# Kernel tuning notes

Hardware: AMD Instinct MI355X
Metric: run time of the kernel (lower is better)

## Reference

```python
import jax, jax.numpy as jnp
import numpy as np

EPS = 1e-5  # BatchNorm eps (torch default); BN is in training mode with gamma=1, beta=0 (init values)


def bn(x, axes):
    m = jnp.mean(x, axis=axes, keepdims=True)
    v = jnp.var(x, axis=axes, keepdims=True)
    return (x - m) * jax.lax.rsqrt(v + EPS)


def knn_idx(xyz, k):
    # brute-force squared-distance matrix [B,N,N], k smallest
    d = jnp.sum((xyz[:, :, None, :] - xyz[:, None, :, :]) ** 2, axis=-1)
    _, idx = jax.lax.top_k(-d, k)
    return idx  # [B,N,k]


def gather(x, idx):
    # x: [B,N,C], idx: [B,N,k] -> [B,N,k,C]
    return jax.vmap(lambda a, i: a[i])(x, idx)


def lse(xyz, features, idx, w):
    nbr_xyz = gather(xyz, idx)                       # [B,N,k,3]
    rel = nbr_xyz - xyz[:, :, None, :]
    dist = jnp.sqrt(jnp.maximum(jnp.sum(rel ** 2, -1, keepdims=True), 1e-12))
    nbr_f = gather(features, idx)                    # [B,N,k,C]
    enc = jnp.concatenate([rel, dist, nbr_f], -1)    # [B,N,k,C+4]
    return jax.nn.relu(bn(jnp.einsum('bnkc,oc->bnko', enc, w), (0, 1, 2)))


def att_pool(x, sw1, sw2, sb2, mw):
    # x: [B,N,k,C]
    h = jax.nn.relu(bn(jnp.einsum('bnkc,oc->bnko', x, sw1), (0, 1, 2)))
    scores = jax.nn.softmax(jnp.einsum('bnkc,oc->bnko', h, sw2) + sb2, axis=2)  # softmax over k
    feat = jnp.sum(x * scores, axis=2)               # [B,N,C]
    return jax.nn.relu(bn(jnp.einsum('bnc,oc->bno', feat, mw), (0, 1)))


def drb(x, w1, w2):
    # in_channels == out_channels -> identity shortcut
    h = jax.nn.relu(bn(jnp.einsum('bnc,oc->bno', x, w1), (0, 1)))
    h = bn(jnp.einsum('bnc,oc->bno', h, w2), (0, 1))
    return jax.nn.relu(h + x)


def setup_inputs() -> dict:
    key = jax.random.key(0)
    B, N, C, K, OUT = 4, 8192, 32, 16, 128
    H = OUT // 2  # 64
    ks = jax.random.split(key, 16)
    s = 0.05
    return {
        'xyz': jax.random.normal(ks[0], (B, N, 3), jnp.float32),
        'features': jax.random.normal(ks[1], (B, N, C), jnp.float32),
        'w_lse1': jax.random.normal(ks[2], (H, C + 4), jnp.float32) * s,
        'w_lse2': jax.random.normal(ks[3], (H, C + 4), jnp.float32) * s,
        'ap1_sw1': jax.random.normal(ks[4], (H, H), jnp.float32) * s,
        'ap1_sw2': jax.random.normal(ks[5], (1, H), jnp.float32) * s,
        'ap1_sb2': jax.random.normal(ks[6], (1,), jnp.float32) * s,
        'ap1_mw': jax.random.normal(ks[7], (H, H), jnp.float32) * s,
        'ap2_sw1': jax.random.normal(ks[8], (H, H), jnp.float32) * s,
        'ap2_sw2': jax.random.normal(ks[9], (1, H), jnp.float32) * s,
        'ap2_sb2': jax.random.normal(ks[10], (1,), jnp.float32) * s,
        'ap2_mw': jax.random.normal(ks[11], (H, H), jnp.float32) * s,
        'drb_w1': jax.random.normal(ks[12], (OUT, OUT), jnp.float32) * s,
        'drb_w2': jax.random.normal(ks[13], (OUT, OUT), jnp.float32) * s,
    }


def reference(xyz, features, w_lse1, w_lse2, ap1_sw1, ap1_sw2, ap1_sb2, ap1_mw,
              ap2_sw1, ap2_sw2, ap2_sb2, ap2_mw, drb_w1, drb_w2):
    K = 16
    idx = knn_idx(xyz, K)  # original calls knn twice on same xyz -> identical indices
    f1 = att_pool(lse(xyz, features, idx, w_lse1), ap1_sw1, ap1_sw2, ap1_sb2, ap1_mw)
    f2 = att_pool(lse(xyz, features, idx, w_lse2), ap2_sw1, ap2_sw2, ap2_sb2, ap2_mw)
    agg = jnp.concatenate([f1, f2], axis=-1)  # [B,N,128]
    return drb(agg, drb_w1, drb_w2)           # [B,N,128]
```

## Files before the change

### kernel.cpp

```cpp
#include <hip/hip_runtime.h>
#include <hip/hip_bf16.h>
#include <hip/hip_fp16.h>
#include <float.h>
#include <math.h>

#define DEVFN __device__ __forceinline__

DEVFN void wavefence() { __builtin_amdgcn_wave_barrier(); }

using half8 = __attribute__((ext_vector_type(8))) _Float16;
using f32x4 = __attribute__((ext_vector_type(4))) float;

namespace {
constexpr int Bq = 4, Nq = 8192, Cq = 32, Kq = 16;
constexpr int PTS = Bq * Nq;
constexpr int CH = 16;
constexpr int CAND = Nq / CH;
constexpr double ROWS = 524288.0;

constexpr int DS_Y = 0, DS_Z = 256, DS_G = 512, DS_H1 = 768, DS_H2 = 1024;

constexpr size_t OFF_KD   = 0;
constexpr size_t OFF_KJ   = (size_t)32 << 20;
constexpr size_t OFF_X    = 0;
constexpr size_t OFF_Z    = (size_t)64 << 20;
constexpr size_t OFF_H1   = 0;
constexpr size_t OFF_H2   = (size_t)16 << 20;
constexpr size_t OFF_GRAW = (size_t)192 << 20;
constexpr size_t OFF_AGG  = (size_t)208 << 20;
constexpr size_t OFF_IDX  = (size_t)224 << 20;
constexpr size_t OFF_DST  = (size_t)226 << 20;
constexpr size_t OFF_MST  = ((size_t)226 << 20) + 10240;
constexpr size_t OFF_BNP  = ((size_t)226 << 20) + 16384;
constexpr size_t WS_NEED  = ((size_t)226 << 20) + 32768;
constexpr size_t FB_GRAW  = (size_t)64 << 20;
constexpr size_t FB_AGG   = (size_t)80 << 20;
constexpr size_t FB_H1    = (size_t)96 << 20;
constexpr size_t FB_H2    = (size_t)112 << 20;
constexpr size_t FB_IDX   = (size_t)128 << 20;
constexpr size_t FB_DST   = (size_t)130 << 20;
constexpr size_t FB_MST   = ((size_t)130 << 20) + 10240;
constexpr size_t FB_BNP   = ((size_t)130 << 20) + 16384;
}

DEVFN void ce_asc(float& a, float& b) {
  const float lo = fminf(a, b), hi = fmaxf(a, b);
  a = lo; b = hi;
}

DEVFN void topk16_update(float* __restrict__ L, float* __restrict__ d) {
#pragma unroll
  for (int k = 2; k <= 16; k <<= 1) {
#pragma unroll
    for (int j = k >> 1; j > 0; j >>= 1) {
#pragma unroll
      for (int i = 0; i < 16; ++i) {
        const int l = i ^ j;
        if (l > i) {
          if ((i & k) == 0) {
            const float lo = fminf(d[i], d[l]), hi = fmaxf(d[i], d[l]);
            d[i] = lo; d[l] = hi;
          } else {
            const float lo = fminf(d[i], d[l]), hi = fmaxf(d[i], d[l]);
            d[i] = hi; d[l] = lo;
          }
        }
      }
    }
  }
#pragma unroll
  for (int i = 0; i < 16; ++i) L[i] = fminf(L[i], d[15 - i]);
#pragma unroll
  for (int j = 8; j > 0; j >>= 1) {
#pragma unroll
    for (int i = 0; i < 16; ++i) {
      const int l = i ^ j;
      if (l > i) ce_asc(L[i], L[l]);
    }
  }
}

DEVFN float distf(const float4 c, const float qx, const float qy, const float qz) {
  const float dx = qx - c.x, dy = qy - c.y, dz = qz - c.z;
  return __fadd_rn(__fadd_rn(__fmul_rn(dx, dx), __fmul_rn(dy, dy)), __fmul_rn(dz, dz));
}

__global__ __launch_bounds__(256, 4) void knn_chunk_kernel(const float* __restrict__ xyz,
                                                           float* __restrict__ pd,
                                                           int* __restrict__ pj) {
  const int b = blockIdx.z;
  const int ch = blockIdx.y;
  const int n = blockIdx.x * 256 + threadIdx.x;
  __shared__ __align__(16) float4 tile[CAND];
  const float* xb = xyz + (size_t)b * Nq * 3;
  for (int t = threadIdx.x; t < CAND; t += 256) {
    const int j = ch * CAND + t;
    tile[t] = make_float4(xb[j * 3], xb[j * 3 + 1], xb[j * 3 + 2], 0.f);
  }
  __syncthreads();
  const float qx = xb[n * 3], qy = xb[n * 3 + 1], qz = xb[n * 3 + 2];
  float L[16];
#pragma unroll
  for (int i = 0; i < 16; ++i) L[i] = FLT_MAX;
  for (int t = 0; t < CAND; t += 16) {
    float d[16];
#pragma unroll
    for (int u = 0; u < 16; ++u) d[u] = distf(tile[t + u], qx, qy, qz);
    topk16_update(L, d);
  }
  const float kth = L[15];
  const size_t base = (((size_t)b * Nq + n) * CH + ch) * Kq;
  int cnt = 0, tfirst = -1;
  for (int t = 0; t < CAND; ++t) {
    const float d = distf(tile[t], qx, qy, qz);
    if (d < kth) { pd[base + cnt] = d; pj[base + cnt] = ch * CAND + t; ++cnt; }
    tfirst = (d == kth && tfirst < 0) ? t : tfirst;
  }
  if (cnt == 15) {
    pd[base + 15] = kth; pj[base + 15] = ch * CAND + tfirst; cnt = 16;
  }
  if (__any(cnt < 16)) {
    for (int t = 0; t < CAND; ++t) {
      const float d = distf(tile[t], qx, qy, qz);
      if (d == kth && cnt < 16) { pd[base + cnt] = d; pj[base + cnt] = ch * CAND + t; ++cnt; }
    }
  }
}

__global__ __launch_bounds__(256, 4) void knn_merge_kernel(const float* __restrict__ pd,
                                                           const int* __restrict__ pj,
                                                           int* __restrict__ idxo) {
  const int q = blockIdx.x * 256 + threadIdx.x;
  const float* dp = pd + (size_t)q * CH * Kq;
  const int* jp = pj + (size_t)q * CH * Kq;
  float L[16];
#pragma unroll
  for (int i = 0; i < 16; ++i) L[i] = FLT_MAX;
  for (int t = 0; t < CH * Kq; t += 16) {
    float d[16];
#pragma unroll
    for (int u = 0; u < 16; u += 4) {
      const float4 v = *(const float4*)(dp + t + u);
      d[u] = v.x; d[u + 1] = v.y; d[u + 2] = v.z; d[u + 3] = v.w;
    }
    topk16_update(L, d);
  }
  const float kth = L[15];
  int* op = idxo + (size_t)q * Kq;
  int cnt = 0;
  for (int t = 0; t < CH * Kq; ++t) {
    const float d = dp[t];
    if (d < kth) { op[cnt] = jp[t]; ++cnt; }
  }
  for (int t = 0; t < CH * Kq; ++t) {
    const float d = dp[t];
    if (d == kth && cnt < 16) { op[cnt] = jp[t]; ++cnt; }
  }
}

struct PF { float4 f0, f1; float nx, ny, nz; };

DEVFN PF issue_feat(const float* __restrict__ features, const float* __restrict__ xyz,
                    int p, int j, int sub) {
  const int b = p >> 13;
  const float* fr = features + ((size_t)b * Nq + j) * Cq;
  const float* xb = xyz + ((size_t)b * Nq + j) * 3;
  PF r;
  r.f0 = *(const float4*)(fr + sub * 8);
  r.f1 = *(const float4*)(fr + sub * 8 + 4);
  r.nx = xb[0]; r.ny = xb[1]; r.nz = xb[2];
  return r;
}

DEVFN int issue_idx(const int* __restrict__ idx, int p, int lane) {
  return idx[(size_t)p * Kq + (lane >> 2)];
}

DEVFN float3 issue_query(const float* __restrict__ xyz, int p) {
  const float* q = xyz + (size_t)p * 3;
  return make_float3(q[0], q[1], q[2]);
}

DEVFN void commit_enc(__half* __restrict__ enc, int lane, const PF& pf,
                      float qx, float qy, float qz) {
  const int k = lane >> 2, sub = lane & 3;
  __half* er = enc + k * 40;
  union { float4 f; __half2 h[4]; } u;
  u.h[0] = __floats2half2_rn(pf.f0.x, pf.f0.y);
  u.h[1] = __floats2half2_rn(pf.f0.z, pf.f0.w);
  u.h[2] = __floats2half2_rn(pf.f1.x, pf.f1.y);
  u.h[3] = __floats2half2_rn(pf.f1.z, pf.f1.w);
  *(float4*)(er + sub * 8) = u.f;
  if (sub == 0) {
    const float rx = pf.nx - qx, ry = pf.ny - qy, rz = pf.nz - qz;
    const float ss = rx * rx + ry * ry + rz * rz;
    const float dd = sqrtf(fmaxf(ss, 1e-12f));
    __half2* rd = (__half2*)(er + 32);
    rd[0] = __floats2half2_rn(rx, ry);
    rd[1] = __floats2half2_rn(rz, dd);
  }
}

DEVFN void commit_enc128(__half* __restrict__ enc, int lane, const PF& pf,
                         float qx, float qy, float qz) {
  const int k = lane >> 2, sub = lane & 3;
  char* base = (char*)enc + k * 128;
  union { float4 f; __half2 h[4]; } u;
  u.h[0] = __floats2half2_rn(pf.f0.x, pf.f0.y);
  u.h[1] = __floats2half2_rn(pf.f0.z, pf.f0.w);
  u.h[2] = __floats2half2_rn(pf.f1.x, pf.f1.y);
  u.h[3] = __floats2half2_rn(pf.f1.z, pf.f1.w);
  *(float4*)(base + ((sub ^ (k & 7)) * 16)) = u.f;
  if (sub == 0) {
    const float rx = pf.nx - qx, ry = pf.ny - qy, rz = pf.nz - qz;
    const float ss = rx * rx + ry * ry + rz * rz;
    const float dd = sqrtf(fmaxf(ss, 1e-12f));
    __half2* aux = (__half2*)(base + ((4 ^ (k & 7)) * 16));
    aux[0] = __floats2half2_rn(rx, ry);
    aux[1] = __floats2half2_rn(rz, dd);
  }
}

DEVFN void zero_enc_pad(__half* __restrict__ enc, int lane) {
  if (lane < 16) {
    const __half2 z2 = __floats2half2_rn(0.f, 0.f);
    __half2* pz = (__half2*)(enc + lane * 40 + 36);
    pz[0] = z2; pz[1] = z2;
  }
}

DEVFN float dot40h(const __half* __restrict__ er, const __half2* __restrict__ wh2) {
  float a0 = 0.f, a1 = 0.f, a2 = 0.f, a3 = 0.f;
#pragma unroll
  for (int r = 0; r < 5; ++r) {
    union { float4 f; __half2 h[4]; } u;
    u.f = *(const float4*)(er + r * 8);
#pragma unroll
    for (int q = 0; q < 4; ++q) {
      const __half2 xv = u.h[q];
      const __half2 wv = wh2[r * 4 + q];
      if (q & 1) {
        a2 += __low2float(xv) * __low2float(wv);
        a3 += __high2float(xv) * __high2float(wv);
      } else {
        a0 += __low2float(xv) * __low2float(wv);
        a1 += __high2float(xv) * __high2float(wv);
      }
    }
  }
  return (a0 + a1) + (a2 + a3);
}

DEVFN float dot64x(const __half* __restrict__ xr, const __half2* __restrict__ sh2) {
  float a0 = 0.f, a1 = 0.f, a2 = 0.f, a3 = 0.f;
#pragma unroll
  for (int r = 0; r < 8; ++r) {
    union { float4 f; __half2 h[4]; } u;
    u.f = *(const float4*)(xr + r * 8);
#pragma unroll
    for (int q = 0; q < 4; ++q) {
      const __half2 xv = u.h[q];
      const __half2 wv = sh2[r * 4 + q];
      if (q & 1) {
        a2 += __low2float(xv) * __low2float(wv);
        a3 += __high2float(xv) * __high2float(wv);
      } else {
        a0 += __low2float(xv) * __low2float(wv);
        a1 += __high2float(xv) * __high2float(wv);
      }
    }
  }
  return (a0 + a1) + (a2 + a3);
}

DEVFN void load_w40(const float* __restrict__ Wrow, __half2* wh2) {
#pragma unroll
  for (int c = 0; c < 16; ++c)
    wh2[c] = __floats2half2_rn(Wrow[4 + 2 * c], Wrow[5 + 2 * c]);
  wh2[16] = __floats2half2_rn(Wrow[0], Wrow[1]);
  wh2[17] = __floats2half2_rn(Wrow[2], Wrow[3]);
  wh2[18] = __floats2half2_rn(0.f, 0.f);
  wh2[19] = wh2[18];
}

DEVFN void load_b1(const float* __restrict__ W, int lane, half8* b1) {
  const int o16 = lane & 15, q = lane >> 4;
#pragma unroll
  for (int t = 0; t < 4; ++t) {
    const int o = t * 16 + o16;
#pragma unroll
    for (int ks = 0; ks < 2; ++ks) {
      half8 v;
#pragma unroll
      for (int j = 0; j < 8; ++j) {
        const int s = ks * 32 + q * 8 + j;
        float wv = 0.f;
        if (s < 36) { const int orig = (s < 32) ? (s + 4) : (s - 32); wv = W[o * 36 + orig]; }
        v[j] = (_Float16)wv;
      }
      b1[t * 2 + ks] = v;
    }
  }
}

DEVFN void load_b2(const float* __restrict__ S1, int lane, half8* b2) {
  const int o16 = lane & 15, q = lane >> 4;
#pragma unroll
  for (int t = 0; t < 4; ++t) {
    const int o = t * 16 + o16;
#pragma unroll
    for (int ks = 0; ks < 2; ++ks) {
      half8 v;
#pragma unroll
      for (int j = 0; j < 8; ++j) {
        const int c = ks * 32 + q * 8 + j;
        v[j] = (_Float16)S1[o * 64 + c];
      }
      b2[t * 2 + ks] = v;
    }
  }
}

#define GATHER_PROLOGUE                                                      \
  int p = wid;                                                               \
  int jc = issue_idx(idx, p, lane);                                          \
  PF cur = issue_feat(features, xyz, p, jc, lane & 3);                       \
  float3 qc = issue_query(xyz, p);                                           \
  int pn0 = p + nw; if (pn0 >= PTS) pn0 = p;                                 \
  int jn = issue_idx(idx, pn0, lane);                                        \
  float3 qn = issue_query(xyz, pn0);                                         \
  for (; p < PTS; p += nw) {                                                 \
    int pn = p + nw; if (pn >= PTS) pn = p;                                  \
    int pn2 = pn + nw; if (pn2 >= PTS) pn2 = pn;                             \
    PF nxt = issue_feat(features, xyz, pn, jn, lane & 3);                    \
    const int jn2 = issue_idx(idx, pn2, lane);                               \
    const float3 q2 = issue_query(xyz, pn2);                                 \
    commit_enc(enc, lane, cur, qc.x, qc.y, qc.z);                            \
    wavefence();

#define GATHER_PROLOGUE_M                                                    \
  int p = wid;                                                               \
  int jc = issue_idx(idx, p, lane);                                          \
  PF cur = issue_feat(features, xyz, p, jc, lane & 3);                       \
  float3 qc = issue_query(xyz, p);                                           \
  int pn0 = p + nw; if (pn0 >= PTS) pn0 = p;                                 \
  int jn = issue_idx(idx, pn0, lane);                                        \
  float3 qn = issue_query(xyz, pn0);                                         \
  for (; p < PTS; p += nw) {                                                 \
    int pn = p + nw; if (pn >= PTS) pn = p;                                  \
    int pn2 = pn + nw; if (pn2 >= PTS) pn2 = pn;                             \
    PF nxt = issue_feat(features, xyz, pn, jn, lane & 3);                    \
    const int jn2 = issue_idx(idx, pn2, lane);                               \
    const float3 q2 = issue_query(xyz, pn2);                                 \
    commit_enc128(enc, lane, cur, qc.x, qc.y, qc.z);                         \
    wavefence();

#define GATHER_EPILOGUE                                                      \
    wavefence();                                                             \
    cur = nxt; qc = qn; qn = q2; jn = jn2;                                   \
  }

__global__ __launch_bounds__(256) void encM_kernel(const float* __restrict__ xyz,
                                                   const float* __restrict__ features,
                                                   const int* __restrict__ idx,
                                                   float* __restrict__ mstat) {
  __shared__ __align__(16) __half encS[4][16 * 40];
  __shared__ float mred[4][36 * 37];
  const int lane = threadIdx.x & 63, wv = threadIdx.x >> 6;
  __half* enc = encS[wv];
  zero_enc_pad(enc, lane);
  wavefence();
  const int li = (lane < 36) ? lane : 0;
  float macc[36];
#pragma unroll
  for (int i = 0; i < 36; ++i) macc[i] = 0.f;
  float vacc = 0.f;
  const int wid = blockIdx.x * 4 + wv, nw = gridDim.x * 4;
  GATHER_PROLOGUE
#pragma unroll
    for (int k = 0; k < 16; ++k) {
      const __half* er = enc + k * 40;
      const float ei = __half2float(er[li]);
      vacc += ei;
#pragma unroll
      for (int r = 0; r < 5; ++r) {
        union { float4 f; __half2 h[4]; } u;
        u.f = *(const float4*)(er + r * 8);
#pragma unroll
        for (int q = 0; q < 4; ++q) {
          const int s = r * 8 + 2 * q;
          if (s < 36)     macc[s]     += ei * __low2float(u.h[q]);
          if (s + 1 < 36) macc[s + 1] += ei * __high2float(u.h[q]);
        }
      }
    }
  GATHER_EPILOGUE
  if (lane < 36) {
#pragma unroll
    for (int j = 0; j < 36; ++j) mred[wv][lane * 37 + j] = macc[j];
    mred[wv][lane * 37 + 36] = vacc;
  }
  __syncthreads();
  for (int t = threadIdx.x; t < 36 * 37; t += 256) {
    const float s = mred[0][t] + mred[1][t] + mred[2][t] + mred[3][t];
    atomicAdd(&mstat[t], s);
  }
}

__global__ void y_finalize_kernel(const float* __restrict__ mstat,
                                  const float* __restrict__ wl1,
                                  const float* __restrict__ wl2,
                                  float* __restrict__ bnp) {
  const int t = threadIdx.x;
  const int br = t >> 6, o = t & 63;
  const float* W = br ? wl2 : wl1;
  double wrow[36];
  for (int s = 0; s < 36; ++s) {
    const int orig = (s < 32) ? (s + 4) : (s - 32);
    wrow[s] = (double)W[o * 36 + orig];
  }
  double mean = 0.0, ey2 = 0.0;
  for (int i = 0; i < 36; ++i) {
    mean += wrow[i] * (double)mstat[i * 37 + 36];
    double rowacc = 0.0;
    for (int j = 0; j < 36; ++j) rowacc += wrow[j] * (double)mstat[i * 37 + j];
    ey2 += wrow[i] * rowacc;
  }
  const double invR = 1.0 / ROWS;
  mean *= invR; ey2 *= invR;
  const double var = ey2 - mean * mean;
  bnp[DS_Y + br * 64 + o] = (float)mean;
  bnp[DS_Y + 128 + br * 64 + o] = (float)(1.0 / sqrt(var + 1e-5));
}

__global__ void bn_finalize_kernel(const double* __restrict__ dstat, float* __restrict__ bnp,
                                   int base, double invc) {
  const int t = threadIdx.x;
  const double m = dstat[base + t] * invc;
  const double v = dstat[base + 128 + t] * invc - m * m;
  bnp[base + t] = (float)m;
  bnp[base + 128 + t] = (float)(1.0 / sqrt(v + 1e-5));
}

__global__ __launch_bounds__(256)
void passA_mat_kernel(const float* __restrict__ xyz,
                      const float* __restrict__ features,
                      const int* __restrict__ idx,
                      const float* __restrict__ wl1,
                      const float* __restrict__ wl2,
                      const float* __restrict__ s1a,
                      const float* __restrict__ s1b,
                      const float* __restrict__ bnp,
                      double* __restrict__ dstat,
                      __half* __restrict__ xbuf,
                      float* __restrict__ zbuf,
                      int br) {
  const float* W = br ? wl2 : wl1;
  const float* S1 = br ? s1b : s1a;
  __shared__ __align__(16) __half encS[4][16 * 64];
  __shared__ __align__(16) __half xS[4][16 * 64];
  const int lane = threadIdx.x & 63, wv = threadIdx.x >> 6;
  __half* enc = encS[wv];
  __half* xL = xS[wv];
  {
    const float4 z4 = {0.f, 0.f, 0.f, 0.f};
    ((float4*)enc)[lane] = z4;
    ((float4*)enc)[lane + 64] = z4;
  }
  wavefence();
  half8 b1[8], b2[8];
  load_b1(W, lane, b1);
  load_b2(S1, lane, b2);
  const int r16 = lane & 15, q4 = lane >> 4;
  float ym4[4], ys4[4];
#pragma unroll
  for (int t = 0; t < 4; ++t) {
    ym4[t] = bnp[DS_Y + br * 64 + t * 16 + r16];
    ys4[t] = bnp[DS_Y + 128 + br * 64 + t * 16 + r16];
  }
  float zs1a[4] = {0.f, 0.f, 0.f, 0.f}, zs2a[4] = {0.f, 0.f, 0.f, 0.f};
  const int wid = blockIdx.x * 4 + wv, nw = gridDim.x * 4;
  GATHER_PROLOGUE_M
    const char* encb = (const char*)enc + r16 * 128;
    const half8 a0 = *(const half8*)(encb + (((q4)     ^ (r16 & 7)) * 16));
    const half8 a1 = *(const half8*)(encb + (((4 + q4) ^ (r16 & 7)) * 16));
    f32x4 yt[4];
#pragma unroll
    for (int t = 0; t < 4; ++t) {
      f32x4 acc = {0.f, 0.f, 0.f, 0.f};
      acc = __builtin_amdgcn_mfma_f32_16x16x32_f16(a0, b1[t * 2], acc, 0, 0, 0);
      acc = __builtin_amdgcn_mfma_f32_16x16x32_f16(a1, b1[t * 2 + 1], acc, 0, 0, 0);
      yt[t] = acc;
    }
#pragma unroll
    for (int t = 0; t < 4; ++t) {
      const int col = t * 16 + r16;
      const int chk = col >> 3;
#pragma unroll
      for (int rr = 0; rr < 4; ++rr) {
        const int row = q4 * 4 + rr;
        float xv = (yt[t][rr] - ym4[t]) * ys4[t];
        xv = xv > 0.f ? xv : 0.f;
        *(_Float16*)((char*)xL + row * 128 + ((chk ^ (row & 7)) * 16) + (col & 7) * 2) =
            (_Float16)xv;
      }
    }
    wavefence();
    const char* xlb = (const char*)xL + r16 * 128;
    const half8 xa0 = *(const half8*)(xlb + (((q4)     ^ (r16 & 7)) * 16));
    const half8 xa1 = *(const half8*)(xlb + (((4 + q4) ^ (r16 & 7)) * 16));
#pragma unroll
    for (int it = 0; it < 2; ++it) {
      const int chunk = it * 64 + lane;
      const int row = chunk >> 3, c8 = chunk & 7;
      const float4 xv4 = *(const float4*)((const char*)xL + row * 128 + ((c8 ^ (row & 7)) * 16));
      *(float4*)((char*)xbuf + (size_t)p * 2048 + chunk * 16) = xv4;
    }
    f32x4 zt[4];
#pragma unroll
    for (int t = 0; t < 4; ++t) {
      f32x4 acc = {0.f, 0.f, 0.f, 0.f};
      acc = __builtin_amdgcn_mfma_f32_16x16x32_f16(xa0, b2[t * 2], acc, 0, 0, 0);
      acc = __builtin_amdgcn_mfma_f32_16x16x32_f16(xa1, b2[t * 2 + 1], acc, 0, 0, 0);
      zt[t] = acc;
    }
#pragma unroll
    for (int t = 0; t < 4; ++t) {
#pragma unroll
      for (int rr = 0; rr < 4; ++rr) {
        const int row = q4 * 4 + rr;
        const float zv = zt[t][rr];
        zbuf[(size_t)p * 1024 + row * 64 + t * 16 + r16] = zv;
        zs1a[t] += zv; zs2a[t] += zv * zv;
      }
    }
  GATHER_EPILOGUE
#pragma unroll
  for (int t = 0; t < 4; ++t) {
    zs1a[t] += __shfl_xor(zs1a[t], 16, 64);
    zs1a[t] += __shfl_xor(zs1a[t], 32, 64);
    zs2a[t] += __shfl_xor(zs2a[t], 16, 64);
    zs2a[t] += __shfl_xor(zs2a[t], 32, 64);
  }
  if (lane < 16) {
#pragma unroll
    for (int t = 0; t < 4; ++t) {
      atomicAdd(&dstat[DS_Z + br * 64 + t * 16 + lane], (double)zs1a[t]);
      atomicAdd(&dstat[DS_Z + 128 + br * 64 + t * 16 + lane], (double)zs2a[t]);
    }
  }
}

__global__ __launch_bounds__(256)
void passB_mat_kernel(const __half* __restrict__ xbuf,
                      const float* __restrict__ zbuf,
                      const float* __restrict__ s2,
                      const float* __restrict__ sb,
                      const float* __restrict__ mw,
                      const float* __restrict__ bnp,
                      double* __restrict__ dstat,
                      float* __restrict__ graw,
                      int br) {
  __shared__ __align__(16) __half2 mwl2[64 * 34];
  __shared__ __align__(16) float featL[4][64];
  for (int t = threadIdx.x; t < 64 * 32; t += 256) {
    const int r = t >> 5, c2 = t & 31;
    mwl2[r * 34 + c2] = __floats2half2_rn(mw[r * 64 + c2 * 2], mw[r * 64 + c2 * 2 + 1]);
  }
  __syncthreads();
  const int lane = threadIdx.x & 63, wv = threadIdx.x >> 6;
  const __half2* mrow = mwl2 + lane * 34;
  const float zm = bnp[DS_Z + br * 64 + lane];
  const float zs = bnp[DS_Z + 128 + br * 64 + lane];
  const float sw2r = s2[lane];
  const float sb2v = sb[0];
  float gs1 = 0.f, gs2 = 0.f;
  const int wid = blockIdx.x * 4 + wv, nw = gridDim.x * 4;
  for (int p = wid; p < PTS; p += nw) {
    const __half* xr = xbuf + (size_t)p * 1024 + lane;
    const float* zr = zbuf + (size_t)p * 1024 + lane;
    float xv[16], pl[16];
#pragma unroll
    for (int k = 0; k < 16; ++k) {
      xv[k] = __half2float(xr[k * 64]);
      float h = (zr[k * 64] - zm) * zs;
      h = h > 0.f ? h : 0.f;
      pl[k] = h * sw2r;
    }
#pragma unroll
    for (int off = 1; off < 64; off <<= 1) {
#pragma unroll
      for (int k = 0; k < 16; ++k) pl[k] += __shfl_xor(pl[k], off, 64);
    }
    float mx = -FLT_MAX;
#pragma unroll
    for (int k = 0; k < 16; ++k) { pl[k] += sb2v; mx = fmaxf(mx, pl[k]); }
    float se = 0.f;
#pragma unroll
    for (int k = 0; k < 16; ++k) { pl[k] = expf(pl[k] - mx); se += pl[k]; }
    const float inv = 1.f / se;
    float f = 0.f;
#pragma unroll
    for (int k = 0; k < 16; ++k) f += xv[k] * (pl[k] * inv);
    featL[wv][lane] = f;
    wavefence();
    const float* featW = &featL[wv][0];
    float g0 = 0.f, g1 = 0.f, g2 = 0.f, g3 = 0.f;
#pragma unroll
    for (int c8 = 0; c8 < 8; ++c8) {
      const float4 fa = *(const float4*)(featW + c8 * 8);
      const float4 fb = *(const float4*)(featW + c8 * 8 + 4);
      const __half2 m0 = mrow[c8 * 4 + 0];
      const __half2 m1 = mrow[c8 * 4 + 1];
      const __half2 m2 = mrow[c8 * 4 + 2];
      const __half2 m3 = mrow[c8 * 4 + 3];
      g0 += fa.x * __low2float(m0); g1 += fa.y * __high2float(m0);
      g2 += fa.z * __low2float(m1); g3 += fa.w * __high2float(m1);
      g0 += fb.x * __low2float(m2); g1 += fb.y * __high2float(m2);
      g2 += fb.z * __low2float(m3); g3 += fb.w * __high2float(m3);
    }
    const float g = (g0 + g1) + (g2 + g3);
    graw[((size_t)br * PTS + p) * 64 + lane] = g;
    gs1 += g; gs2 += g * g;
    wavefence();
  }
  atomicAdd(&dstat[DS_G + br * 64 + lane], (double)gs1);
  atomicAdd(&dstat[DS_G + 128 + br * 64 + lane], (double)gs2);
}

__global__ __launch_bounds__(256)
void passA_kernel(const float* __restrict__ xyz,
                  const float* __restrict__ features,
                  const int* __restrict__ idx,
                  const float* __restrict__ wl1,
                  const float* __restrict__ wl2,
                  const float* __restrict__ s1a,
                  const float* __restrict__ s1b,
                  const float* __restrict__ bnp,
                  double* __restrict__ dstat) {
  const int br = blockIdx.y;
  const float* W = br ? wl2 : wl1;
  const float* S1 = br ? s1b : s1a;
  __shared__ __align__(16) __half encS[4][16 * 40];
  __shared__ __align__(16) __half xS[4][16 * 64];
  const int lane = threadIdx.x & 63, wv = threadIdx.x >> 6;
  __half* enc = encS[wv];
  __half* xL = xS[wv];
  zero_enc_pad(enc, lane);
  wavefence();
  __half2 wh2[20];
  load_w40(W + lane * 36, wh2);
  __half2 sh2[32];
#pragma unroll
  for (int c = 0; c < 32; ++c)
    sh2[c] = __floats2half2_rn(S1[lane * 64 + 2 * c], S1[lane * 64 + 2 * c + 1]);
  const float ym = bnp[DS_Y + br * 64 + lane];
  const float ys = bnp[DS_Y + 128 + br * 64 + lane];
  float zs1 = 0.f, zs2 = 0.f;
  const int wid = blockIdx.x * 4 + wv, nw = gridDim.x * 4;
  GATHER_PROLOGUE
#pragma unroll
    for (int k = 0; k < 16; ++k) {
      float xv = (dot40h(enc + k * 40, wh2) - ym) * ys;
      xv = xv > 0.f ? xv : 0.f;
      xL[k * 64 + lane] = __float2half(xv);
    }
    wavefence();
#pragma unroll
    for (int k = 0; k < 16; ++k) {
      const float acc = dot64x(xL + k * 64, sh2);
      zs1 += acc; zs2 += acc * acc;
    }
  GATHER_EPILOGUE
  atomicAdd(&dstat[DS_Z + br * 64 + lane], (double)zs1);
  atomicAdd(&dstat[DS_Z + 128 + br * 64 + lane], (double)zs2);
}

__global__ __launch_bounds__(256)
void passB_kernel(const float* __restrict__ xyz,
                  const float* __restrict__ features,
                  const int* __restrict__ idx,
                  const float* __restrict__ wl1,
                  const float* __restrict__ wl2,
                  const float* __restrict__ s1a,
                  const float* __restrict__ s1b,
                  const float* __restrict__ s2a,
                  const float* __restrict__ s2b,
                  const float* __restrict__ sba,
                  const float* __restrict__ sbb,
                  const float* __restrict__ mwa,
                  const float* __restrict__ mwb,
                  const float* __restrict__ bnp,
                  double* __restrict__ dstat,
                  float* __restrict__ graw) {
  const int br = blockIdx.y;
  const float* W = br ? wl2 : wl1;
  const float* S1 = br ? s1b : s1a;
  const float* S2 = br ? s2b : s2a;
  const float* SB = br ? sbb : sba;
  const float* MW = br ? mwb : mwa;
  __shared__ __align__(16) __half2 mwl2[64 * 34];
  __shared__ __align__(16) __half encS[4][16 * 40];
  __shared__ __align__(16) __half xS[4][16 * 64];
  __shared__ __align__(16) float featL[4][64];
  for (int t = threadIdx.x; t < 64 * 32; t += 256) {
    const int r = t >> 5, c2 = t & 31;
    mwl2[r * 34 + c2] = __floats2half2_rn(MW[r * 64 + c2 * 2], MW[r * 64 + c2 * 2 + 1]);
  }
  __syncthreads();
  const int lane = threadIdx.x & 63, wv = threadIdx.x >> 6;
  __half* enc = encS[wv];
  __half* xL = xS[wv];
  zero_enc_pad(enc, lane);
  wavefence();
  const __half2* mrow = mwl2 + lane * 34;
  __half2 wh2[20];
  load_w40(W + lane * 36, wh2);
  __half2 sh2[32];
#pragma unroll
  for (int c = 0; c < 32; ++c)
    sh2[c] = __floats2half2_rn(S1[lane * 64 + 2 * c], S1[lane * 64 + 2 * c + 1]);
  const float ym = bnp[DS_Y + br * 64 + lane];
  const float ys = bnp[DS_Y + 128 + br * 64 + lane];
  const float zm = bnp[DS_Z + br * 64 + lane];
  const float zs = bnp[DS_Z + 128 + br * 64 + lane];
  const float sw2r = S2[lane];
  const float sb2v = SB[0];
  float gs1 = 0.f, gs2 = 0.f;
  const int wid = blockIdx.x * 4 + wv, nw = gridDim.x * 4;
  GATHER_PROLOGUE
#pragma unroll
    for (int k = 0; k < 16; ++k) {
      float xv = (dot40h(enc + k * 40, wh2) - ym) * ys;
      xv = xv > 0.f ? xv : 0.f;
      xL[k * 64 + lane] = __float2half(xv);
    }
    wavefence();
    float pl[16];
#pragma unroll
    for (int k = 0; k < 16; ++k) {
      float h = (dot64x(xL + k * 64, sh2) - zm) * zs;
      h = h > 0.f ? h : 0.f;
      pl[k] = h * sw2r;
    }
#pragma unroll
    for (int off = 1; off < 64; off <<= 1) {
#pragma unroll
      for (int k = 0; k < 16; ++k) pl[k] += __shfl_xor(pl[k], off, 64);
    }
    float mx = -FLT_MAX;
#pragma unroll
    for (int k = 0; k < 16; ++k) { pl[k] += sb2v; mx = fmaxf(mx, pl[k]); }
    float se = 0.f;
#pragma unroll
    for (int k = 0; k < 16; ++k) { pl[k] = expf(pl[k] - mx); se += pl[k]; }
    const float inv = 1.f / se;
    float f = 0.f;
#pragma unroll
    for (int k = 0; k < 16; ++k) f += __half2float(xL[k * 64 + lane]) * (pl[k] * inv);
    featL[wv][lane] = f;
    wavefence();
    const float* featW = &featL[wv][0];
    float g0 = 0.f, g1 = 0.f, g2 = 0.f, g3 = 0.f;
#pragma unroll
    for (int c8 = 0; c8 < 8; ++c8) {
      const float4 fa = *(const float4*)(featW + c8 * 8);
      const float4 fb = *(const float4*)(featW + c8 * 8 + 4);
      const __half2 m0 = mrow[c8 * 4 + 0];
      const __half2 m1 = mrow[c8 * 4 + 1];
      const __half2 m2 = mrow[c8 * 4 + 2];
      const __half2 m3 = mrow[c8 * 4 + 3];
      g0 += fa.x * __low2float(m0); g1 += fa.y * __high2float(m0);
      g2 += fa.z * __low2float(m1); g3 += fa.w * __high2float(m1);
      g0 += fb.x * __low2float(m2); g1 += fb.y * __high2float(m2);
      g2 += fb.z * __low2float(m3); g3 += fb.w * __high2float(m3);
    }
    const float g = (g0 + g1) + (g2 + g3);
    graw[((size_t)br * PTS + p) * 64 + lane] = g;
    gs1 += g; gs2 += g * g;
  GATHER_EPILOGUE
  atomicAdd(&dstat[DS_G + br * 64 + lane], (double)gs1);
  atomicAdd(&dstat[DS_G + 128 + br * 64 + lane], (double)gs2);
}

__global__ __launch_bounds__(256) void drb_mm_kernel(const float* __restrict__ in,
                                                     const float* __restrict__ wmat,
                                                     const float* __restrict__ bnp,
                                                     double* __restrict__ dstat,
                                                     float* __restrict__ aggout,
                                                     float* __restrict__ rowout,
                                                     int bpIn, int dsOut, int mode) {
  __shared__ __align__(16) float wlds[128 * 129];
  __shared__ __align__(16) float rowS[4][128];
  for (int t = threadIdx.x; t < 128 * 128; t += 256) wlds[(t >> 7) * 129 + (t & 127)] = wmat[t];
  __syncthreads();
  const int lane = threadIdx.x & 63, wv = threadIdx.x >> 6;
  const float m0 = bnp[bpIn + lane], s0 = bnp[bpIn + 128 + lane];
  const float m1 = bnp[bpIn + 64 + lane], s1 = bnp[bpIn + 128 + 64 + lane];
  float a1s0 = 0.f, a1s1 = 0.f, a2s0 = 0.f, a2s1 = 0.f;
  const int wid = blockIdx.x * 4 + wv, nw = gridDim.x * 4;
  for (int p = wid; p < PTS; p += nw) {
    float v0, v1;
    if (mode == 0) {
      v0 = in[(size_t)p * 64 + lane];
      v1 = in[(size_t)PTS * 64 + (size_t)p * 64 + lane];
    } else {
      v0 = in[(size_t)p * 128 + lane];
      v1 = in[(size_t)p * 128 + 64 + lane];
    }
    v0 = (v0 - m0) * s0; v0 = v0 > 0.f ? v0 : 0.f;
    v1 = (v1 - m1) * s1; v1 = v1 > 0.f ? v1 : 0.f;
    rowS[wv][lane] = v0;
    rowS[wv][64 + lane] = v1;
    if (aggout) {
      aggout[(size_t)p * 128 + lane] = v0;
      aggout[(size_t)p * 128 + 64 + lane] = v1;
    }
    wavefence();
#pragma unroll
    for (int h = 0; h < 2; ++h) {
      const int o = h * 64 + lane;
      float b0 = 0.f, b1 = 0.f, b2 = 0.f, b3 = 0.f;
#pragma unroll
      for (int c4 = 0; c4 < 32; ++c4) {
        const float4 rv = *(const float4*)(&rowS[wv][c4 * 4]);
        b0 += rv.x * wlds[o * 129 + c4 * 4 + 0];
        b1 += rv.y * wlds[o * 129 + c4 * 4 + 1];
        b2 += rv.z * wlds[o * 129 + c4 * 4 + 2];
        b3 += rv.w * wlds[o * 129 + c4 * 4 + 3];
      }
      const float acc = (b0 + b1) + (b2 + b3);
      rowout[(size_t)p * 128 + o] = acc;
      if (h == 0) { a1s0 += acc; a2s0 += acc * acc; }
      else        { a1s1 += acc; a2s1 += acc * acc; }
    }
    wavefence();
  }
  atomicAdd(&dstat[dsOut + lane], (double)a1s0);
  atomicAdd(&dstat[dsOut + 64 + lane], (double)a1s1);
  atomicAdd(&dstat[dsOut + 128 + lane], (double)a2s0);
  atomicAdd(&dstat[dsOut + 128 + 64 + lane], (double)a2s1);
}

__global__ __launch_bounds__(256) void final_kernel(const float* __restrict__ h2,
                                                    const float* __restrict__ agg,
                                                    const float* __restrict__ bnp,
                                                    float* __restrict__ out) {
  const size_t e = (size_t)blockIdx.x * 256 + threadIdx.x;
  const int ch = (int)(e & 127);
  const float m = bnp[DS_H2 + ch], s = bnp[DS_H2 + 128 + ch];
  float v = (h2[e] - m) * s + agg[e];
  out[e] = v > 0.f ? v : 0.f;
}

extern "C" void kernel_launch(void* const* d_in, const int* in_sizes, int n_in,
                              void* d_out, int out_size, void* d_ws, size_t ws_size,
                              hipStream_t stream) {
  (void)in_sizes; (void)n_in; (void)out_size;
  const float* xyz      = (const float*)d_in[0];
  const float* features = (const float*)d_in[1];
  const float* w_lse1   = (const float*)d_in[2];
  const float* w_lse2   = (const float*)d_in[3];
  const float* ap1_sw1  = (const float*)d_in[4];
  const float* ap1_sw2  = (const float*)d_in[5];
  const float* ap1_sb2  = (const float*)d_in[6];
  const float* ap1_mw   = (const float*)d_in[7];
  const float* ap2_sw1  = (const float*)d_in[8];
  const float* ap2_sw2  = (const float*)d_in[9];
  const float* ap2_sb2  = (const float*)d_in[10];
  const float* ap2_mw   = (const float*)d_in[11];
  const float* drb_w1   = (const float*)d_in[12];
  const float* drb_w2   = (const float*)d_in[13];

  char* ws = (char*)d_ws;
  const bool mat = (ws_size >= WS_NEED);

  float*  knn_d = (float*)(ws + OFF_KD);
  int*    knn_j = (int*)(ws + OFF_KJ);
  int*    idx   = (int*)(ws + (mat ? OFF_IDX : FB_IDX));
  double* dstat = (double*)(ws + (mat ? OFF_DST : FB_DST));
  float*  mstat = (float*)(ws + (mat ? OFF_MST : FB_MST));
  float*  bnp   = (float*)(ws + (mat ? OFF_BNP : FB_BNP));
  float*  graw  = (float*)(ws + (mat ? OFF_GRAW : FB_GRAW));
  float*  agg   = (float*)(ws + (mat ? OFF_AGG : FB_AGG));
  float*  h1    = (float*)(ws + (mat ? OFF_H1 : FB_H1));
  float*  h2    = (float*)(ws + (mat ? OFF_H2 : FB_H2));
  float*  out   = (float*)d_out;

  (void)hipMemsetAsync(dstat, 0, 1280 * sizeof(double) + 36 * 37 * sizeof(float), stream);

  knn_chunk_kernel<<<dim3(Nq / 256, CH, Bq), 256, 0, stream>>>(xyz, knn_d, knn_j);
  knn_merge_kernel<<<dim3(PTS / 256), 256, 0, stream>>>(knn_d, knn_j, idx);

  encM_kernel<<<dim3(1280), 256, 0, stream>>>(xyz, features, idx, mstat);
  y_finalize_kernel<<<1, 128, 0, stream>>>(mstat, w_lse1, w_lse2, bnp);

  if (mat) {
    __half* xbuf = (__half*)(ws + OFF_X);
    float*  zbuf = (float*)(ws + OFF_Z);
    for (int br = 0; br < 2; ++br) {
      passA_mat_kernel<<<dim3(1280), 256, 0, stream>>>(xyz, features, idx, w_lse1, w_lse2,
                                                       ap1_sw1, ap2_sw1, bnp, dstat,
                                                       xbuf, zbuf, br);
      bn_finalize_kernel<<<1, 128, 0, stream>>>(dstat, bnp, DS_Z, 1.0 / ROWS);
      passB_mat_kernel<<<dim3(1024), 256, 0, stream>>>(xbuf, zbuf,
                                                       br ? ap2_sw2 : ap1_sw2,
                                                       br ? ap2_sb2 : ap1_sb2,
                                                       br ? ap2_mw : ap1_mw,
                                                       bnp, dstat, graw, br);
    }
  } else {
    passA_kernel<<<dim3(640, 2), 256, 0, stream>>>(xyz, features, idx, w_lse1, w_lse2,
                                                   ap1_sw1, ap2_sw1, bnp, dstat);
    bn_finalize_kernel<<<1, 128, 0, stream>>>(dstat, bnp, DS_Z, 1.0 / ROWS);
    passB_kernel<<<dim3(512, 2), 256, 0, stream>>>(xyz, features, idx, w_lse1, w_lse2,
                                                   ap1_sw1, ap2_sw1, ap1_sw2, ap2_sw2,
                                                   ap1_sb2, ap2_sb2, ap1_mw, ap2_mw,
                                                   bnp, dstat, graw);
  }
  bn_finalize_kernel<<<1, 128, 0, stream>>>(dstat, bnp, DS_G, 1.0 / PTS);

  drb_mm_kernel<<<dim3(512), 256, 0, stream>>>(graw, drb_w1, bnp, dstat, agg, h1,
                                               DS_G, DS_H1, 0);
  bn_finalize_kernel<<<1, 128, 0, stream>>>(dstat, bnp, DS_H1, 1.0 / PTS);

  drb_mm_kernel<<<dim3(512), 256, 0, stream>>>(h1, drb_w2, bnp, dstat, nullptr, h2,
                                               DS_H1, DS_H2, 1);
  bn_finalize_kernel<<<1, 128, 0, stream>>>(dstat, bnp, DS_H2, 1.0 / PTS);

  final_kernel<<<dim3(PTS * 128 / 256), 256, 0, stream>>>(h2, agg, bnp, out);
}
```

Measured before the change: 1.348 ms.

## Fuse both branch gathers into one pass and recompute z instead of storing it

Pass A now gathers neighbours once and writes the fp16 post-BN activations for both branches, which removes the second gather pass. The fp32 z buffer, which cost a 64 MB write and read per branch, is gone. A new zstat kernel re-reads x for both branches to collect the z BatchNorm statistics with MFMA, and pass B recomputes z through MFMA into shared memory before the softmax pooling. This trades extra x reads and recomputed matmuls for less global traffic and one fewer gather.

```diff
diff --git a/kernel.cpp b/kernel.cpp
--- a/kernel.cpp
+++ b/kernel.cpp
@@ -22,8 +22,8 @@
 
 constexpr size_t OFF_KD   = 0;
 constexpr size_t OFF_KJ   = (size_t)32 << 20;
-constexpr size_t OFF_X    = 0;
-constexpr size_t OFF_Z    = (size_t)64 << 20;
+constexpr size_t OFF_X0   = 0;
+constexpr size_t OFF_X1   = (size_t)64 << 20;
 constexpr size_t OFF_H1   = 0;
 constexpr size_t OFF_H2   = (size_t)16 << 20;
 constexpr size_t OFF_GRAW = (size_t)192 << 20;
@@ -443,20 +443,14 @@
 }
 
 __global__ __launch_bounds__(256)
-void passA_mat_kernel(const float* __restrict__ xyz,
-                      const float* __restrict__ features,
-                      const int* __restrict__ idx,
-                      const float* __restrict__ wl1,
-                      const float* __restrict__ wl2,
-                      const float* __restrict__ s1a,
-                      const float* __restrict__ s1b,
-                      const float* __restrict__ bnp,
-                      double* __restrict__ dstat,
-                      __half* __restrict__ xbuf,
-                      float* __restrict__ zbuf,
-                      int br) {
-  const float* W = br ? wl2 : wl1;
-  const float* S1 = br ? s1b : s1a;
+void passA2_mat_kernel(const float* __restrict__ xyz,
+                       const float* __restrict__ features,
+                       const int* __restrict__ idx,
+                       const float* __restrict__ wl1,
+                       const float* __restrict__ wl2,
+                       const float* __restrict__ bnp,
+                       __half* __restrict__ x0buf,
+                       __half* __restrict__ x1buf) {
   __shared__ __align__(16) __half encS[4][16 * 64];
   __shared__ __align__(16) __half xS[4][16 * 64];
   const int lane = threadIdx.x & 63, wv = threadIdx.x >> 6;
@@ -468,122 +462,190 @@
     ((float4*)enc)[lane + 64] = z4;
   }
   wavefence();
-  half8 b1[8], b2[8];
-  load_b1(W, lane, b1);
-  load_b2(S1, lane, b2);
+  half8 b1a[8], b1b[8];
+  load_b1(wl1, lane, b1a);
+  load_b1(wl2, lane, b1b);
   const int r16 = lane & 15, q4 = lane >> 4;
-  float ym4[4], ys4[4];
+  float ym0[4], ys0[4], ym1[4], ys1[4];
 #pragma unroll
   for (int t = 0; t < 4; ++t) {
-    ym4[t] = bnp[DS_Y + br * 64 + t * 16 + r16];
-    ys4[t] = bnp[DS_Y + 128 + br * 64 + t * 16 + r16];
-  }
-  float zs1a[4] = {0.f, 0.f, 0.f, 0.f}, zs2a[4] = {0.f, 0.f, 0.f, 0.f};
+    ym0[t] = bnp[DS_Y + t * 16 + r16];
+    ys0[t] = bnp[DS_Y + 128 + t * 16 + r16];
+    ym1[t] = bnp[DS_Y + 64 + t * 16 + r16];
+    ys1[t] = bnp[DS_Y + 128 + 64 + t * 16 + r16];
+  }
   const int wid = blockIdx.x * 4 + wv, nw = gridDim.x * 4;
   GATHER_PROLOGUE_M
     const char* encb = (const char*)enc + r16 * 128;
     const half8 a0 = *(const half8*)(encb + (((q4)     ^ (r16 & 7)) * 16));
     const half8 a1 = *(const half8*)(encb + (((4 + q4) ^ (r16 & 7)) * 16));
-    f32x4 yt[4];
+    {
+      f32x4 yt[4];
+#pragma unroll
+      for (int t = 0; t < 4; ++t) {
+        f32x4 acc = {0.f, 0.f, 0.f, 0.f};
+        acc = __builtin_amdgcn_mfma_f32_16x16x32_f16(a0, b1a[t * 2], acc, 0, 0, 0);
+        acc = __builtin_amdgcn_mfma_f32_16x16x32_f16(a1, b1a[t * 2 + 1], acc, 0, 0, 0);
+        yt[t] = acc;
+      }
+#pragma unroll
+      for (int t = 0; t < 4; ++t) {
+        const int col = t * 16 + r16;
+        const int chk = col >> 3;
+#pragma unroll
+        for (int rr = 0; rr < 4; ++rr) {
+          const int row = q4 * 4 + rr;
+          float xv = (yt[t][rr] - ym0[t]) * ys0[t];
+          xv = xv > 0.f ? xv : 0.f;
+          *(_Float16*)((char*)xL + row * 128 + ((chk ^ (row & 7)) * 16) + (col & 7) * 2) =
+              (_Float16)xv;
+        }
+      }
+      wavefence();
+#pragma unroll
+      for (int it = 0; it < 2; ++it) {
+        const int chunk = it * 64 + lane;
+        const int row = chunk >> 3, c8 = chunk & 7;
+        const float4 xv4 = *(const float4*)((const char*)xL + row * 128 + ((c8 ^ (row & 7)) * 16));
+        *(float4*)((char*)x0buf + (size_t)p * 2048 + chunk * 16) = xv4;
+      }
+      wavefence();
+    }
+    {
+      f32x4 yt[4];
+#pragma unroll
+      for (int t = 0; t < 4; ++t) {
+        f32x4 acc = {0.f, 0.f, 0.f, 0.f};
+        acc = __builtin_amdgcn_mfma_f32_16x16x32_f16(a0, b1b[t * 2], acc, 0, 0, 0);
+        acc = __builtin_amdgcn_mfma_f32_16x16x32_f16(a1, b1b[t * 2 + 1], acc, 0, 0, 0);
+        yt[t] = acc;
+      }
+#pragma unroll
+      for (int t = 0; t < 4; ++t) {
+        const int col = t * 16 + r16;
+        const int chk = col >> 3;
+#pragma unroll
+        for (int rr = 0; rr < 4; ++rr) {
+          const int row = q4 * 4 + rr;
+          float xv = (yt[t][rr] - ym1[t]) * ys1[t];
+          xv = xv > 0.f ? xv : 0.f;
+          *(_Float16*)((char*)xL + row * 128 + ((chk ^ (row & 7)) * 16) + (col & 7) * 2) =
+              (_Float16)xv;
+        }
+      }
+      wavefence();
+#pragma unroll
+      for (int it = 0; it < 2; ++it) {
+        const int chunk = it * 64 + lane;
+        const int row = chunk >> 3, c8 = chunk & 7;
+        const float4 xv4 = *(const float4*)((const char*)xL + row * 128 + ((c8 ^ (row & 7)) * 16));
+        *(float4*)((char*)x1buf + (size_t)p * 2048 + chunk * 16) = xv4;
+      }
+    }
+  GATHER_EPILOGUE
+}
+
+__global__ __launch_bounds__(256)
+void zstat_kernel(const __half* __restrict__ x0, const __half* __restrict__ x1,
+                  const float* __restrict__ s1a, const float* __restrict__ s1b,
+                  double* __restrict__ dstat) {
+  const int lane = threadIdx.x & 63, wv = threadIdx.x >> 6;
+  half8 b2a[8], b2b[8];
+  load_b2(s1a, lane, b2a);
+  load_b2(s1b, lane, b2b);
+  const int r16 = lane & 15, q4 = lane >> 4;
+  float sa1[4] = {0.f, 0.f, 0.f, 0.f}, sa2[4] = {0.f, 0.f, 0.f, 0.f};
+  float sb1[4] = {0.f, 0.f, 0.f, 0.f}, sb2s[4] = {0.f, 0.f, 0.f, 0.f};
+  const int wid = blockIdx.x * 4 + wv, nw = gridDim.x * 4;
+  for (int p = wid; p < PTS; p += nw) {
+    const size_t abase = (size_t)p * 1024 + r16 * 64 + q4 * 8;
+    const half8 xa0 = *(const half8*)(x0 + abase);
+    const half8 xa1 = *(const half8*)(x0 + abase + 32);
+    const half8 xb0 = *(const half8*)(x1 + abase);
+    const half8 xb1 = *(const half8*)(x1 + abase + 32);
 #pragma unroll
     for (int t = 0; t < 4; ++t) {
       f32x4 acc = {0.f, 0.f, 0.f, 0.f};
-      acc = __builtin_amdgcn_mfma_f32_16x16x32_f16(a0, b1[t * 2], acc, 0, 0, 0);
-      acc = __builtin_amdgcn_mfma_f32_16x16x32_f16(a1, b1[t * 2 + 1], acc, 0, 0, 0);
-      yt[t] = acc;
-    }
+      acc = __builtin_amdgcn_mfma_f32_16x16x32_f16(xa0, b2a[t * 2], acc, 0, 0, 0);
+      acc = __builtin_amdgcn_mfma_f32_16x16x32_f16(xa1, b2a[t * 2 + 1], acc, 0, 0, 0);
+#pragma unroll
+      for (int rr = 0; rr < 4; ++rr) { const float zv = acc[rr]; sa1[t] += zv; sa2[t] += zv * zv; }
+      f32x4 acc2 = {0.f, 0.f, 0.f, 0.f};
+      acc2 = __builtin_amdgcn_mfma_f32_16x16x32_f16(xb0, b2b[t * 2], acc2, 0, 0, 0);
+      acc2 = __builtin_amdgcn_mfma_f32_16x16x32_f16(xb1, b2b[t * 2 + 1], acc2, 0, 0, 0);
+#pragma unroll
+      for (int rr = 0; rr < 4; ++rr) { const float zv = acc2[rr]; sb1[t] += zv; sb2s[t] += zv * zv; }
+    }
+  }
+#pragma unroll
+  for (int t = 0; t < 4; ++t) {
+    sa1[t] += __shfl_xor(sa1[t], 16, 64);  sa1[t] += __shfl_xor(sa1[t], 32, 64);
+    sa2[t] += __shfl_xor(sa2[t], 16, 64);  sa2[t] += __shfl_xor(sa2[t], 32, 64);
+    sb1[t] += __shfl_xor(sb1[t], 16, 64);  sb1[t] += __shfl_xor(sb1[t], 32, 64);
+    sb2s[t] += __shfl_xor(sb2s[t], 16, 64); sb2s[t] += __shfl_xor(sb2s[t], 32, 64);
+  }
+  if (lane < 16) {
 #pragma unroll
     for (int t = 0; t < 4; ++t) {
-      const int col = t * 16 + r16;
-      const int chk = col >> 3;
-#pragma unroll
-      for (int rr = 0; rr < 4; ++rr) {
-        const int row = q4 * 4 + rr;
-        float xv = (yt[t][rr] - ym4[t]) * ys4[t];
-        xv = xv > 0.f ? xv : 0.f;
-        *(_Float16*)((char*)xL + row * 128 + ((chk ^ (row & 7)) * 16) + (col & 7) * 2) =
-            (_Float16)xv;
-      }
-    }
-    wavefence();
-    const char* xlb = (const char*)xL + r16 * 128;
-    const half8 xa0 = *(const half8*)(xlb + (((q4)     ^ (r16 & 7)) * 16));
-    const half8 xa1 = *(const half8*)(xlb + (((4 + q4) ^ (r16 & 7)) * 16));
-#pragma unroll
-    for (int it = 0; it < 2; ++it) {
-      const int chunk = it * 64 + lane;
-      const int row = chunk >> 3, c8 = chunk & 7;
-      const float4 xv4 = *(const float4*)((const char*)xL + row * 128 + ((c8 ^ (row & 7)) * 16));
-      *(float4*)((char*)xbuf + (size_t)p * 2048 + chunk * 16) = xv4;
-    }
-    f32x4 zt[4];
+      atomicAdd(&dstat[DS_Z + t * 16 + lane], (double)sa1[t]);
+      atomicAdd(&dstat[DS_Z + 128 + t * 16 + lane], (double)sa2[t]);
+      atomicAdd(&dstat[DS_Z + 64 + t * 16 + lane], (double)sb1[t]);
+      atomicAdd(&dstat[DS_Z + 128 + 64 + t * 16 + lane], (double)sb2s[t]);
+    }
+  }
+}
+
+__global__ __launch_bounds__(256)
+void passB2_mat_kernel(const __half* __restrict__ xbuf,
+                       const float* __restrict__ S1,
+                       const float* __restrict__ s2,
+                       const float* __restrict__ sb,
+                       const float* __restrict__ mw,
+                       const float* __restrict__ bnp,
+                       double* __restrict__ dstat,
+                       float* __restrict__ graw,
+                       int br) {
+  __shared__ __align__(16) __half2 mwl2[64 * 34];
+  __shared__ __align__(16) float featL[4][64];
+  __shared__ __align__(16) float zS[4][16 * 64];
+  for (int t = threadIdx.x; t < 64 * 32; t += 256) {
+    const int r = t >> 5, c2 = t & 31;
+    mwl2[r * 34 + c2] = __floats2half2_rn(mw[r * 64 + c2 * 2], mw[r * 64 + c2 * 2 + 1]);
+  }
+  __syncthreads();
+  const int lane = threadIdx.x & 63, wv = threadIdx.x >> 6;
+  const int r16 = lane & 15, q4 = lane >> 4;
+  half8 b2[8];
+  load_b2(S1, lane, b2);
+  const __half2* mrow = mwl2 + lane * 34;
+  const float zm = bnp[DS_Z + br * 64 + lane];
+  const float zsc = bnp[DS_Z + 128 + br * 64 + lane];
+  const float sw2r = s2[lane];
+  const float sb2v = sb[0];
+  float gs1 = 0.f, gs2 = 0.f;
+  float* zw = &zS[wv][0];
+  const int wid = blockIdx.x * 4 + wv, nw = gridDim.x * 4;
+  for (int p = wid; p < PTS; p += nw) {
+    const size_t abase = (size_t)p * 1024 + r16 * 64 + q4 * 8;
+    const half8 xa0 = *(const half8*)(xbuf + abase);
+    const half8 xa1 = *(const half8*)(xbuf + abase + 32);
 #pragma unroll
     for (int t = 0; t < 4; ++t) {
       f32x4 acc = {0.f, 0.f, 0.f, 0.f};
       acc = __builtin_amdgcn_mfma_f32_16x16x32_f16(xa0, b2[t * 2], acc, 0, 0, 0);
       acc = __builtin_amdgcn_mfma_f32_16x16x32_f16(xa1, b2[t * 2 + 1], acc, 0, 0, 0);
-      zt[t] = acc;
-    }
-#pragma unroll
-    for (int t = 0; t < 4; ++t) {
-#pragma unroll
-      for (int rr = 0; rr < 4; ++rr) {
-        const int row = q4 * 4 + rr;
-        const float zv = zt[t][rr];
-        zbuf[(size_t)p * 1024 + row * 64 + t * 16 + r16] = zv;
-        zs1a[t] += zv; zs2a[t] += zv * zv;
-      }
-    }
-  GATHER_EPILOGUE
-#pragma unroll
-  for (int t = 0; t < 4; ++t) {
-    zs1a[t] += __shfl_xor(zs1a[t], 16, 64);
-    zs1a[t] += __shfl_xor(zs1a[t], 32, 64);
-    zs2a[t] += __shfl_xor(zs2a[t], 16, 64);
-    zs2a[t] += __shfl_xor(zs2a[t], 32, 64);
-  }
-  if (lane < 16) {
-#pragma unroll
-    for (int t = 0; t < 4; ++t) {
-      atomicAdd(&dstat[DS_Z + br * 64 + t * 16 + lane], (double)zs1a[t]);
-      atomicAdd(&dstat[DS_Z + 128 + br * 64 + t * 16 + lane], (double)zs2a[t]);
-    }
-  }
-}
-
-__global__ __launch_bounds__(256)
-void passB_mat_kernel(const __half* __restrict__ xbuf,
-                      const float* __restrict__ zbuf,
-                      const float* __restrict__ s2,
-                      const float* __restrict__ sb,
-                      const float* __restrict__ mw,
-                      const float* __restrict__ bnp,
-                      double* __restrict__ dstat,
-                      float* __restrict__ graw,
-                      int br) {
-  __shared__ __align__(16) __half2 mwl2[64 * 34];
-  __shared__ __align__(16) float featL[4][64];
-  for (int t = threadIdx.x; t < 64 * 32; t += 256) {
-    const int r = t >> 5, c2 = t & 31;
-    mwl2[r * 34 + c2] = __floats2half2_rn(mw[r * 64 + c2 * 2], mw[r * 64 + c2 * 2 + 1]);
-  }
-  __syncthreads();
-  const int lane = threadIdx.x & 63, wv = threadIdx.x >> 6;
-  const __half2* mrow = mwl2 + lane * 34;
-  const float zm = bnp[DS_Z + br * 64 + lane];
-  const float zs = bnp[DS_Z + 128 + br * 64 + lane];
-  const float sw2r = s2[lane];
-  const float sb2v = sb[0];
-  float gs1 = 0.f, gs2 = 0.f;
-  const int wid = blockIdx.x * 4 + wv, nw = gridDim.x * 4;
-  for (int p = wid; p < PTS; p += nw) {
+#pragma unroll
+      for (int rr = 0; rr < 4; ++rr)
+        zw[(q4 * 4 + rr) * 64 + t * 16 + r16] = acc[rr];
+    }
+    wavefence();
     const __half* xr = xbuf + (size_t)p * 1024 + lane;
-    const float* zr = zbuf + (size_t)p * 1024 + lane;
+    const float* zr = zw + lane;
     float xv[16], pl[16];
 #pragma unroll
     for (int k = 0; k < 16; ++k) {
       xv[k] = __half2float(xr[k * 64]);
-      float h = (zr[k * 64] - zm) * zs;
+      float h = (zr[k * 64] - zm) * zsc;
       h = h > 0.f ? h : 0.f;
       pl[k] = h * sw2r;
     }
@@ -896,19 +958,16 @@
   y_finalize_kernel<<<1, 128, 0, stream>>>(mstat, w_lse1, w_lse2, bnp);
 
   if (mat) {
-    __half* xbuf = (__half*)(ws + OFF_X);
-    float*  zbuf = (float*)(ws + OFF_Z);
-    for (int br = 0; br < 2; ++br) {
-      passA_mat_kernel<<<dim3(1280), 256, 0, stream>>>(xyz, features, idx, w_lse1, w_lse2,
-                                                       ap1_sw1, ap2_sw1, bnp, dstat,
-                                                       xbuf, zbuf, br);
-      bn_finalize_kernel<<<1, 128, 0, stream>>>(dstat, bnp, DS_Z, 1.0 / ROWS);
-      passB_mat_kernel<<<dim3(1024), 256, 0, stream>>>(xbuf, zbuf,
-                                                       br ? ap2_sw2 : ap1_sw2,
-                                                       br ? ap2_sb2 : ap1_sb2,
-                                                       br ? ap2_mw : ap1_mw,
-                                                       bnp, dstat, graw, br);
-    }
+    __half* x0 = (__half*)(ws + OFF_X0);
+    __half* x1 = (__half*)(ws + OFF_X1);
+    passA2_mat_kernel<<<dim3(1280), 256, 0, stream>>>(xyz, features, idx, w_lse1, w_lse2,
+                                                      bnp, x0, x1);
+    zstat_kernel<<<dim3(1024), 256, 0, stream>>>(x0, x1, ap1_sw1, ap2_sw1, dstat);
+    bn_finalize_kernel<<<1, 128, 0, stream>>>(dstat, bnp, DS_Z, 1.0 / ROWS);
+    passB2_mat_kernel<<<dim3(1024), 256, 0, stream>>>(x0, ap1_sw1, ap1_sw2, ap1_sb2,
+                                                      ap1_mw, bnp, dstat, graw, 0);
+    passB2_mat_kernel<<<dim3(1024), 256, 0, stream>>>(x1, ap2_sw1, ap2_sw2, ap2_sb2,
+                                                      ap2_mw, bnp, dstat, graw, 1);
   } else {
     passA_kernel<<<dim3(640, 2), 256, 0, stream>>>(xyz, features, idx, w_lse1, w_lse2,
                                                    ap1_sw1, ap2_sw1, bnp, dstat);
```

After: 1.259 ms. 1.07x faster.
